# Performance work log

Hardware: AMD Instinct MI355X
Metric: run time of the kernel (lower is better)

Reference implementation:

```python
import jax, jax.numpy as jnp
import numpy as np

K = 3          # conv kernel size
G = 3          # KAN grid intervals
SPLINE_K = 3   # B-spline order
N_BASIS = G + SPLINE_K  # 6


def extended_grid():
    # pykan-style grid on [-1, 1] with G intervals, extended by k knots each side
    h = 2.0 / G
    return jnp.arange(-SPLINE_K, G + SPLINE_K + 1, dtype=jnp.float32) * h - 1.0  # [G+2k+1]


def bspline_basis(x, t, k):
    """Cox-de Boor recursion. x: [...], t: [m] knots -> [..., m-1-k] bases."""
    x = x[..., None]
    b = ((x >= t[:-1]) & (x < t[1:])).astype(x.dtype)  # degree 0: [..., m-1]
    for d in range(1, k + 1):
        left = (x - t[: -(d + 1)]) / (t[d:-1] - t[: -(d + 1)]) * b[..., :-1]
        right = (t[d + 1:] - x) / (t[d + 1:] - t[1:-d]) * b[..., 1:]
        b = left + right
    return b  # [..., m-1-k]


def setup_inputs() -> dict:
    key = jax.random.key(0)
    k1, k2, k3, k4 = jax.random.split(key, 4)
    B, C, H, W = 32, 16, 64, 64
    in_dim, out_dim = C * K * K, 64
    x = jax.random.normal(k1, (B, C, H, W), dtype=jnp.float32)
    coef = jax.random.normal(k2, (in_dim, out_dim, N_BASIS), dtype=jnp.float32) * 0.1
    scale_base = jax.random.normal(k3, (in_dim, out_dim), dtype=jnp.float32) * (1.0 / np.sqrt(in_dim))
    scale_sp = jnp.ones((in_dim, out_dim), dtype=jnp.float32) + 0.0 * jax.random.normal(k4, (in_dim, out_dim))
    return {"x": x, "coef": coef, "scale_base": scale_base, "scale_sp": scale_sp}


def reference(x, coef, scale_base, scale_sp):
    B, C, H, W = x.shape
    Ho, Wo = H - K + 1, W - K + 1
    # im2col with torch-reshape ordering: feature index = c*K*K + di*K + dj
    cols = [x[:, :, di:di + Ho, dj:dj + Wo] for di in range(K) for dj in range(K)]
    patches = jnp.stack(cols, axis=2)                    # [B, C, K*K, Ho, Wo]
    patches = patches.reshape(B, C * K * K, Ho, Wo)      # [B, D, Ho, Wo]
    p = patches.transpose(0, 2, 3, 1)                    # [B, Ho, Wo, D]

    t = extended_grid()
    basis = bspline_basis(p, t, SPLINE_K)                # [B, Ho, Wo, D, N_BASIS]
    # spline part: sum over input dims and bases, with per-edge scale_sp folded into coef
    spline = jnp.einsum('bhwdn,don->bhwo', basis, coef * scale_sp[:, :, None])
    base = jnp.einsum('bhwd,do->bhwo', jax.nn.silu(p), scale_base)
    y = base + spline                                    # [B, Ho, Wo, O]
    return y.transpose(0, 3, 1, 2)                       # [B, O, Ho, Wo]
```

## Files before the change

kernel.cpp:

```cpp
#include <hip/hip_runtime.h>
#include <math.h>

#define Bsz 32
#define Cc  16
#define Hh  64
#define Ww  64
#define HO  62
#define WO  62
#define OD  64
#define ND  144
#define NCHUNK 36
#define BSKEW 520
#define BSM_U16 77824

using short8 = __attribute__((ext_vector_type(8))) short;
using f32x4  = __attribute__((ext_vector_type(4))) float;

__device__ __forceinline__ unsigned short f2bf(float f) {
    union { float f; unsigned u; } v; v.f = f;
    unsigned r = v.u + 0x7fff + ((v.u >> 16) & 1);
    return (unsigned short)(r >> 16);
}
__device__ __forceinline__ float bf2f(unsigned short h) {
    union { unsigned u; float f; } v; v.u = ((unsigned)h) << 16; return v.f;
}

__device__ __forceinline__ uint4 feat_pack(float xv) {
    float xi = (xv + 3.0f) * 1.5f;
    float fi = floorf(xi);
    int   ii = (int)fi;
    float u  = xi - fi;
    float u2 = u * u, u3 = u2 * u;
    float P0 = u3 * (1.0f / 6.0f);
    float P1 = (1.0f + 3.0f * u + 3.0f * u2 - 3.0f * u3) * (1.0f / 6.0f);
    float P2 = (4.0f - 6.0f * u2 + 3.0f * u3) * (1.0f / 6.0f);
    float om = 1.0f - u;
    float P3 = om * om * om * (1.0f / 6.0f);
    bool ok = (ii >= 0) && (ii <= 8);
    float bas[6];
    #pragma unroll
    for (int n = 0; n < 6; ++n) {
        int t = ii - n;
        float v = (t == 0) ? P0 : (t == 1) ? P1 : (t == 2) ? P2 : (t == 3) ? P3 : 0.0f;
        bas[n] = ok ? v : 0.0f;
    }
    float s = xv / (1.0f + __expf(-xv));
    unsigned short sh = f2bf(s);
    unsigned short sl = f2bf(s - bf2f(sh));
    uint4 pk;
    pk.x = (unsigned)f2bf(bas[0]) | ((unsigned)f2bf(bas[1]) << 16);
    pk.y = (unsigned)f2bf(bas[2]) | ((unsigned)f2bf(bas[3]) << 16);
    pk.z = (unsigned)f2bf(bas[4]) | ((unsigned)f2bf(bas[5]) << 16);
    pk.w = (unsigned)sh | ((unsigned)sl << 16);
    return pk;
}

__global__ __launch_bounds__(256) void kan_feat(const float* __restrict__ x,
                                                uint4* __restrict__ fg) {
    int base = blockIdx.x * 2048 + threadIdx.x;
    #pragma unroll
    for (int j = 0; j < 8; ++j) {
        int i = base + j * 256;
        fg[i] = feat_pack(x[i]);
    }
}

__global__ __launch_bounds__(256) void kan_prep2(const float* __restrict__ coef,
                                                 const float* __restrict__ sbase,
                                                 const float* __restrict__ ssp,
                                                 unsigned short* __restrict__ wps) {
    int p = blockIdx.x * 256 + threadIdx.x;
    if (p >= BSM_U16) return;
    int dd  = p / BSKEW;
    int rem = p - dd * BSKEW;
    int o = rem >> 3, n = rem & 7;
    float v = 0.0f;
    if (dd < ND && rem < 512)
        v = (n < 6) ? coef[(dd * OD + o) * 6 + n] * ssp[dd * OD + o] : sbase[dd * OD + o];
    wps[p] = f2bf(v);
}

__global__ __launch_bounds__(512) void kan_gemm(const uint4* __restrict__ fg,
                                                const unsigned short* __restrict__ wps,
                                                float* __restrict__ out) {
    __shared__ unsigned short bsm[BSM_U16];

    const int tid  = threadIdx.x;
    const int bb   = blockIdx.x >> 3;
    const int h    = (blockIdx.x & 7) * 8 + (tid >> 6);
    const int wid  = tid >> 6;
    const int lane = tid & 63;
    const int l15  = lane & 15;
    const int ks   = lane >> 4;
    const bool alive = (h < HO);

    {
        const uint4* src = (const uint4*)wps;
        uint4* dst = (uint4*)bsm;
        #pragma unroll
        for (int it = 0; it < 19; ++it) dst[it * 512 + tid] = src[it * 512 + tid];
    }
    __syncthreads();

    f32x4 acc[4][4];
    #pragma unroll
    for (int rt = 0; rt < 4; ++rt)
        #pragma unroll
        for (int ct = 0; ct < 4; ++ct) acc[rt][ct] = (f32x4){0.f, 0.f, 0.f, 0.f};

    if (alive) {
        const unsigned short* bbase = bsm + ks * BSKEW + l15 * 8;

        auto loadA = [&](int cb, short8* A) {
            int dd  = cb * 4 + ks;
            int c   = (dd * 57) >> 9;
            int rem = dd - c * 9;
            int di  = (rem * 11) >> 5;
            int dj  = rem - di * 3;
            const short8* ap = (const short8*)fg + ((((bb * Cc + c) << 6) + h + di) << 6) + l15 + dj;
            A[0] = ap[0]; A[1] = ap[16]; A[2] = ap[32]; A[3] = ap[48];
        };
        auto loadB = [&](int cb, short8* Bf) {
            const short8* bp = (const short8*)(bbase + cb * 4 * BSKEW);
            Bf[0] = bp[0]; Bf[1] = bp[16]; Bf[2] = bp[32]; Bf[3] = bp[48];
        };

        short8 A0[4], B0[4], A1[4], B1[4];
        loadA(0, A0); loadB(0, B0);
        for (int cb = 0; cb < NCHUNK; cb += 2) {
            loadA(cb + 1, A1); loadB(cb + 1, B1);
            #pragma unroll
            for (int rt = 0; rt < 4; ++rt)
                #pragma unroll
                for (int ct = 0; ct < 4; ++ct)
                    acc[rt][ct] = __builtin_amdgcn_mfma_f32_16x16x32_bf16(A0[rt], B0[ct], acc[rt][ct], 0, 0, 0);
            if (cb + 2 < NCHUNK) { loadA(cb + 2, A0); loadB(cb + 2, B0); }
            #pragma unroll
            for (int rt = 0; rt < 4; ++rt)
                #pragma unroll
                for (int ct = 0; ct < 4; ++ct)
                    acc[rt][ct] = __builtin_amdgcn_mfma_f32_16x16x32_bf16(A1[rt], B1[ct], acc[rt][ct], 0, 0, 0);
        }
    }

    __syncthreads();
    if (alive) {
        float* sc = (float*)bsm + wid * (OD * 68);
        #pragma unroll
        for (int rt = 0; rt < 4; ++rt)
            #pragma unroll
            for (int ct = 0; ct < 4; ++ct)
                *(f32x4*)&sc[(ct * 16 + l15) * 68 + rt * 16 + ks * 4] = acc[rt][ct];
        #pragma unroll 4
        for (int j = 0; j < OD; ++j) {
            float v = sc[j * 68 + lane];
            if (lane < WO) out[((bb * OD + j) * HO + h) * WO + lane] = v;
        }
    }
}

#define FW 68
__global__ __launch_bounds__(256) void kan_prep(const float* __restrict__ coef,
                                                const float* __restrict__ sbase,
                                                const float* __restrict__ ssp,
                                                unsigned short* __restrict__ wp) {
    int idx = blockIdx.x * 256 + threadIdx.x;
    if (idx >= ND * OD * 8) return;
    int n = idx & 7, o = (idx >> 3) & 63, d = idx >> 9;
    float v = (n < 6) ? coef[(d * OD + o) * 6 + n] * ssp[d * OD + o] : sbase[d * OD + o];
    wp[idx] = f2bf(v);
}

__global__ __launch_bounds__(128) void kan_mfma(const float* __restrict__ x,
                                                const unsigned short* __restrict__ wp,
                                                float* __restrict__ out) {
    __shared__ uint4 feat[Cc * 4 * FW];
    const int rp = blockIdx.x, b = blockIdx.y, tid = threadIdx.x;
    const int wid = tid >> 6, lane = tid & 63, l15 = lane & 15, ks = lane >> 4;
    const int hrow0 = rp * 2;
    for (int i = tid; i < Cc * 4 * FW; i += 128) {
        int wl = i % FW, cr = i / FW, r = cr & 3, c = cr >> 2;
        int col = wl < Ww ? wl : Ww - 1;
        feat[i] = feat_pack(x[((b * Cc + c) * Hh + hrow0 + r) * Ww + col]);
    }
    __syncthreads();
    f32x4 acc[4][4];
    #pragma unroll
    for (int rt = 0; rt < 4; ++rt)
        #pragma unroll
        for (int ct = 0; ct < 4; ++ct) acc[rt][ct] = (f32x4){0.f, 0.f, 0.f, 0.f};
    auto loadA = [&](int chunk, short8* A) {
        int d = chunk * 4 + ks;
        int c = (d * 57) >> 9;
        int rem = d - c * 9;
        int di = (rem * 11) >> 5;
        int dj = rem - di * 3;
        const short8* ap = (const short8*)&feat[(c * 4 + wid + di) * FW + l15 + dj];
        A[0] = ap[0]; A[1] = ap[16]; A[2] = ap[32]; A[3] = ap[48];
    };
    auto loadB = [&](int chunk, short8* Bf) {
        int d = chunk * 4 + ks;
        const short8* bp = (const short8*)wp + (d * 64 + l15);
        Bf[0] = bp[0]; Bf[1] = bp[16]; Bf[2] = bp[32]; Bf[3] = bp[48];
    };
    short8 A0[4], B0[4], A1[4], B1[4];
    loadA(0, A0); loadB(0, B0);
    for (int cb = 0; cb < NCHUNK; cb += 2) {
        loadA(cb + 1, A1); loadB(cb + 1, B1);
        #pragma unroll
        for (int rt = 0; rt < 4; ++rt)
            #pragma unroll
            for (int ct = 0; ct < 4; ++ct)
                acc[rt][ct] = __builtin_amdgcn_mfma_f32_16x16x32_bf16(A0[rt], B0[ct], acc[rt][ct], 0, 0, 0);
        if (cb + 2 < NCHUNK) { loadA(cb + 2, A0); loadB(cb + 2, B0); }
        #pragma unroll
        for (int rt = 0; rt < 4; ++rt)
            #pragma unroll
            for (int ct = 0; ct < 4; ++ct)
                acc[rt][ct] = __builtin_amdgcn_mfma_f32_16x16x32_bf16(A1[rt], B1[ct], acc[rt][ct], 0, 0, 0);
    }
    __syncthreads();
    float* sC = ((float*)feat) + wid * (OD * FW);
    #pragma unroll
    for (int rt = 0; rt < 4; ++rt)
        #pragma unroll
        for (int ct = 0; ct < 4; ++ct)
            *(f32x4*)&sC[(ct * 16 + l15) * FW + rt * 16 + ks * 4] = acc[rt][ct];
    const int orow = hrow0 + wid;
    for (int j = 0; j < OD; ++j) {
        float v = sC[j * FW + lane];
        if (lane < WO) out[((b * OD + j) * HO + orow) * WO + lane] = v;
    }
}

extern "C" void kernel_launch(void* const* d_in, const int* in_sizes, int n_in,
                              void* d_out, int out_size, void* d_ws, size_t ws_size,
                              hipStream_t stream) {
    (void)in_sizes; (void)n_in; (void)out_size;
    const float* x     = (const float*)d_in[0];
    const float* coef  = (const float*)d_in[1];
    const float* sbase = (const float*)d_in[2];
    const float* ssp   = (const float*)d_in[3];
    float* out = (float*)d_out;

    const size_t wps_bytes  = (size_t)BSM_U16 * 2;
    const size_t featg_bytes = (size_t)Bsz * Cc * Hh * Ww * 16;
    const size_t need = wps_bytes + featg_bytes + 64;

    if (ws_size >= need) {
        unsigned short* wps = (unsigned short*)d_ws;
        uint4* fg = (uint4*)((char*)d_ws + wps_bytes);
        kan_feat<<<1024, 256, 0, stream>>>(x, fg);
        kan_prep2<<<(BSM_U16 + 255) / 256, 256, 0, stream>>>(coef, sbase, ssp, wps);
        kan_gemm<<<256, 512, 0, stream>>>(fg, wps, out);
    } else if (ws_size >= (size_t)ND * OD * 8 * 2) {
        unsigned short* wp = (unsigned short*)d_ws;
        kan_prep<<<(ND * OD * 8 + 255) / 256, 256, 0, stream>>>(coef, sbase, ssp, wp);
        dim3 grid(HO / 2, Bsz);
        kan_mfma<<<grid, 128, 0, stream>>>(x, wp, out);
    }
}
```

Measured before the change: 48.29 us.

## Merge feature and weight prep kernels, deepen A prefetch, vectorize output stores

The separate feature-packing and weight-prep kernels become one launch, with blocks split by index, which removes one kernel launch and its gap. The feature path now reads x as float4, four values per thread. The GEMM main loop goes from double-buffered to triple-buffered A-fragment loads with double-buffered B, so global loads have more lead time before their MFMAs. The epilogue writes output rows as float2 across two half-waves instead of scalar stores. Costs are more live registers for the extra A buffers and a less straightforward write pattern in the feature kernel.

```diff
diff --git a/kernel.cpp b/kernel.cpp
--- a/kernel.cpp
+++ b/kernel.cpp
@@ -56,28 +56,46 @@
 }
 
 __global__ __launch_bounds__(256) void kan_feat(const float* __restrict__ x,
-                                                uint4* __restrict__ fg) {
-    int base = blockIdx.x * 2048 + threadIdx.x;
-    #pragma unroll
-    for (int j = 0; j < 8; ++j) {
-        int i = base + j * 256;
-        fg[i] = feat_pack(x[i]);
-    }
-}
-
-__global__ __launch_bounds__(256) void kan_prep2(const float* __restrict__ coef,
-                                                 const float* __restrict__ sbase,
-                                                 const float* __restrict__ ssp,
-                                                 unsigned short* __restrict__ wps) {
-    int p = blockIdx.x * 256 + threadIdx.x;
-    if (p >= BSM_U16) return;
-    int dd  = p / BSKEW;
-    int rem = p - dd * BSKEW;
-    int o = rem >> 3, n = rem & 7;
-    float v = 0.0f;
-    if (dd < ND && rem < 512)
-        v = (n < 6) ? coef[(dd * OD + o) * 6 + n] * ssp[dd * OD + o] : sbase[dd * OD + o];
-    wps[p] = f2bf(v);
+                                                const float* __restrict__ coef,
+                                                const float* __restrict__ sbase,
+                                                const float* __restrict__ ssp,
+                                                uint4* __restrict__ fg,
+                                                unsigned short* __restrict__ wps) {
+    const int bid = blockIdx.x, tid = threadIdx.x;
+    if (bid < 1024) {
+        #pragma unroll
+        for (int p = 0; p < 2; ++p) {
+            int e0 = bid * 2048 + p * 1024 + tid * 4;
+            float4 xv = *(const float4*)&x[e0];
+            fg[e0 + 0] = feat_pack(xv.x);
+            fg[e0 + 1] = feat_pack(xv.y);
+            fg[e0 + 2] = feat_pack(xv.z);
+            fg[e0 + 3] = feat_pack(xv.w);
+        }
+    } else {
+        int g = (bid - 1024) * 256 + tid;
+        if (g >= BSM_U16 / 8) return;
+        int p8   = g * 8;
+        int dd   = p8 / BSKEW;
+        int rem8 = (p8 - dd * BSKEW) >> 3;
+        unsigned short v8[8];
+        #pragma unroll
+        for (int n = 0; n < 8; ++n) v8[n] = 0;
+        if (dd < ND && rem8 < 64) {
+            int o = rem8;
+            float sspv = ssp[dd * OD + o];
+            #pragma unroll
+            for (int n = 0; n < 6; ++n) v8[n] = f2bf(coef[(dd * OD + o) * 6 + n] * sspv);
+            unsigned short sb = f2bf(sbase[dd * OD + o]);
+            v8[6] = sb; v8[7] = sb;
+        }
+        uint4 pk;
+        pk.x = (unsigned)v8[0] | ((unsigned)v8[1] << 16);
+        pk.y = (unsigned)v8[2] | ((unsigned)v8[3] << 16);
+        pk.z = (unsigned)v8[4] | ((unsigned)v8[5] << 16);
+        pk.w = (unsigned)v8[6] | ((unsigned)v8[7] << 16);
+        *(uint4*)&wps[p8] = pk;
+    }
 }
 
 __global__ __launch_bounds__(512) void kan_gemm(const uint4* __restrict__ fg,
@@ -87,8 +105,8 @@
 
     const int tid  = threadIdx.x;
     const int bb   = blockIdx.x >> 3;
-    const int h    = (blockIdx.x & 7) * 8 + (tid >> 6);
     const int wid  = tid >> 6;
+    const int h    = (blockIdx.x & 7) * 8 + wid;
     const int lane = tid & 63;
     const int l15  = lane & 15;
     const int ks   = lane >> 4;
@@ -124,22 +142,37 @@
             const short8* bp = (const short8*)(bbase + cb * 4 * BSKEW);
             Bf[0] = bp[0]; Bf[1] = bp[16]; Bf[2] = bp[32]; Bf[3] = bp[48];
         };
-
-        short8 A0[4], B0[4], A1[4], B1[4];
-        loadA(0, A0); loadB(0, B0);
-        for (int cb = 0; cb < NCHUNK; cb += 2) {
-            loadA(cb + 1, A1); loadB(cb + 1, B1);
+        auto mfmas = [&](short8* Ax, short8* Bx) {
             #pragma unroll
             for (int rt = 0; rt < 4; ++rt)
                 #pragma unroll
                 for (int ct = 0; ct < 4; ++ct)
-                    acc[rt][ct] = __builtin_amdgcn_mfma_f32_16x16x32_bf16(A0[rt], B0[ct], acc[rt][ct], 0, 0, 0);
-            if (cb + 2 < NCHUNK) { loadA(cb + 2, A0); loadB(cb + 2, B0); }
-            #pragma unroll
-            for (int rt = 0; rt < 4; ++rt)
-                #pragma unroll
-                for (int ct = 0; ct < 4; ++ct)
-                    acc[rt][ct] = __builtin_amdgcn_mfma_f32_16x16x32_bf16(A1[rt], B1[ct], acc[rt][ct], 0, 0, 0);
+                    acc[rt][ct] = __builtin_amdgcn_mfma_f32_16x16x32_bf16(Ax[rt], Bx[ct], acc[rt][ct], 0, 0, 0);
+        };
+
+        short8 A0[4], A1[4], A2[4], B0[4], B1[4];
+        loadA(0, A0); loadA(1, A1); loadA(2, A2);
+        loadB(0, B0); loadB(1, B1);
+
+        for (int cb = 0; cb < NCHUNK; cb += 6) {
+            mfmas(A0, B0);
+            if (cb + 3 < NCHUNK) loadA(cb + 3, A0);
+            if (cb + 2 < NCHUNK) loadB(cb + 2, B0);
+            mfmas(A1, B1);
+            if (cb + 4 < NCHUNK) loadA(cb + 4, A1);
+            if (cb + 3 < NCHUNK) loadB(cb + 3, B1);
+            mfmas(A2, B0);
+            if (cb + 5 < NCHUNK) loadA(cb + 5, A2);
+            if (cb + 4 < NCHUNK) loadB(cb + 4, B0);
+            mfmas(A0, B1);
+            if (cb + 6 < NCHUNK) loadA(cb + 6, A0);
+            if (cb + 5 < NCHUNK) loadB(cb + 5, B1);
+            mfmas(A1, B0);
+            if (cb + 7 < NCHUNK) loadA(cb + 7, A1);
+            if (cb + 6 < NCHUNK) loadB(cb + 6, B0);
+            mfmas(A2, B1);
+            if (cb + 8 < NCHUNK) loadA(cb + 8, A2);
+            if (cb + 7 < NCHUNK) loadB(cb + 7, B1);
         }
     }
 
@@ -151,10 +184,16 @@
             #pragma unroll
             for (int ct = 0; ct < 4; ++ct)
                 *(f32x4*)&sc[(ct * 16 + l15) * 68 + rt * 16 + ks * 4] = acc[rt][ct];
-        #pragma unroll 4
-        for (int j = 0; j < OD; ++j) {
-            float v = sc[j * 68 + lane];
-            if (lane < WO) out[((bb * OD + j) * HO + h) * WO + lane] = v;
+
+        const int jh = lane >> 5;
+        const int r  = lane & 31;
+        #pragma unroll 8
+        for (int it = 0; it < 32; ++it) {
+            int j = it * 2 + jh;
+            if (r < 31) {
+                float2 v = *(float2*)&sc[j * 68 + r * 2];
+                *(float2*)&out[((bb * OD + j) * HO + h) * WO + r * 2] = v;
+            }
         }
     }
 }
@@ -243,15 +282,14 @@
     const float* ssp   = (const float*)d_in[3];
     float* out = (float*)d_out;
 
-    const size_t wps_bytes  = (size_t)BSM_U16 * 2;
+    const size_t wps_bytes   = (size_t)BSM_U16 * 2;
     const size_t featg_bytes = (size_t)Bsz * Cc * Hh * Ww * 16;
     const size_t need = wps_bytes + featg_bytes + 64;
 
     if (ws_size >= need) {
         unsigned short* wps = (unsigned short*)d_ws;
         uint4* fg = (uint4*)((char*)d_ws + wps_bytes);
-        kan_feat<<<1024, 256, 0, stream>>>(x, fg);
-        kan_prep2<<<(BSM_U16 + 255) / 256, 256, 0, stream>>>(coef, sbase, ssp, wps);
+        kan_feat<<<1024 + 38, 256, 0, stream>>>(x, coef, sbase, ssp, fg, wps);
         kan_gemm<<<256, 512, 0, stream>>>(fg, wps, out);
     } else if (ws_size >= (size_t)ND * OD * 8 * 2) {
         unsigned short* wp = (unsigned short*)d_ws;
```

Result: slower. 54.65 us (+13.2%).
